# Kernel tuning notes

Hardware: AMD Instinct MI355X
Metric: run time of the kernel (lower is better)

The kernel has to match this reference:

```python
import jax, jax.numpy as jnp
import numpy as np


def _chamfer_sq(points, gts):
    # points: [B,N,3], gts: [B,M,3]
    pn = jnp.sum(points * points, axis=-1)              # [B,N]
    gn = jnp.sum(gts * gts, axis=-1)                    # [B,M]
    cross = jnp.einsum('bnd,bmd->bnm', points, gts)     # [B,N,M]
    d = pn[:, :, None] + gn[:, None, :] - 2.0 * cross   # [B,N,M]
    d = jnp.maximum(d, 0.0)
    p2g = jnp.min(d, axis=2)                            # [B,N] squared NN dist
    g2p = jnp.min(d, axis=1)                            # [B,M]
    return p2g, g2p


def setup_inputs() -> dict:
    key = jax.random.key(0)
    k1, k2 = jax.random.split(key)
    B, N, M = 8, 4096, 4096
    points = jax.random.normal(k1, (B, N, 3), dtype=jnp.float32)
    gts = jax.random.normal(k2, (B, M, 3), dtype=jnp.float32)
    return {"points": points, "gts": gts}


def reference(points, gts):
    p2g_sq, g2p_sq = _chamfer_sq(points, gts)
    p2g = jnp.sqrt(jnp.mean(p2g_sq, axis=1))   # [B]
    g2p = jnp.sqrt(jnp.mean(g2p_sq, axis=1))   # [B]
    loss = (p2g + g2p) / 2.0
    return (jnp.mean(loss), jnp.mean(p2g), jnp.mean(g2p))
```

## Files before the change

kernel.cpp:

```cpp
#include <hip/hip_runtime.h>
#include <math.h>

#define NPTS 4096
#define NB   8
#define QCB  512
#define RCB  1024
#define NQC  (NPTS / QCB)
#define NRC  (NPTS / RCB)

typedef _Float16 h8     __attribute__((ext_vector_type(8)));
typedef float    f32x16 __attribute__((ext_vector_type(16)));

#define FOREACH_T(OP) OP(0) OP(1) OP(2) OP(3)

__device__ __forceinline__ void split2(float v, _Float16& h, _Float16& l) {
    h = (_Float16)v;
    l = (_Float16)(v - (float)h);
}

__global__ __launch_bounds__(256, 2) void chamfer_mfma32(
    const float* __restrict__ P, const float* __restrict__ G,
    float* __restrict__ qpart,
    float* __restrict__ rpart,
    int* __restrict__ counter)
{
    __shared__ __align__(16) unsigned char smem[32768];
    h8*    Bfr = (h8*)smem;
    float* qtr = (float*)smem;

    const int dir = blockIdx.z;
    const int b   = blockIdx.y;
    const int qc  = blockIdx.x >> 2;
    const int rc  = blockIdx.x & 3;
    const int tid = threadIdx.x;
    const int w    = tid >> 6;
    const int lane = tid & 63;
    const int col  = lane & 31;
    const int kg   = lane >> 5;

    if (blockIdx.x == 0 && b == 0 && dir == 0 && tid == 0) *counter = 0;

    const float* __restrict__ Qb = (dir ? G : P) + (size_t)b * NPTS * 3;
    const float* __restrict__ Rb = (dir ? P : G) + (size_t)b * NPTS * 3;

    const _Float16 one = (_Float16)1.f, zr = (_Float16)0.f;

#pragma unroll
    for (int i = 0; i < 8; ++i) {
        const int e    = tid + i * 256;
        const int el   = e & 63;
        const int ecol = el & 31, ekg = el >> 5;
        const int ref  = rc * RCB + (e >> 6) * 32 + ecol;
        const float gx = Rb[3 * ref], gy = Rb[3 * ref + 1], gz = Rb[3 * ref + 2];
        const float gn = fmaf(gx, gx, fmaf(gy, gy, gz * gz));
        _Float16 xh, xl, yh, yl, zh, zl, nh, nl;
        split2(gx, xh, xl); split2(gy, yh, yl); split2(gz, zh, zl); split2(gn, nh, nl);
        Bfr[e] = ekg ? (h8){one, nh, xl, yl, zl, zr, nl, zr}
                     : (h8){xh, yh, zh, one, nh, xh, yh, zh};
    }

#define DECLT(t) h8 afr##t; f32x16 qa##t;
    FOREACH_T(DECLT)
#undef DECLT
#define MKA(t) { \
        const int q0 = qc * QCB + w * 128 + (t) * 32 + col;                   \
        const float px = Qb[3 * q0], py = Qb[3 * q0 + 1], pz = Qb[3 * q0 + 2];\
        const float m2x = -2.f * px, m2y = -2.f * py, m2z = -2.f * pz;        \
        const float pn = fmaf(px, px, fmaf(py, py, pz * pz));                 \
        _Float16 xh, xl, yh, yl, zh, zl, ph, pl;                              \
        split2(m2x, xh, xl); split2(m2y, yh, yl); split2(m2z, zh, zl);        \
        split2(pn, ph, pl);                                                   \
        afr##t = kg ? (h8){pl, zr, xh, yh, zh, ph, one, zr}                   \
                    : (h8){xh, yh, zh, ph, one, xl, yl, zl};                  \
        _Pragma("unroll")                                                     \
        for (int j = 0; j < 16; ++j) qa##t[j] = 3.4e38f; }
    FOREACH_T(MKA)
#undef MKA

    __syncthreads();

    const f32x16 cz = (f32x16){0.f,0.f,0.f,0.f,0.f,0.f,0.f,0.f,
                               0.f,0.f,0.f,0.f,0.f,0.f,0.f,0.f};
#pragma unroll 2
    for (int rt = 0; rt < 32; ++rt) {
        const h8 bfr = Bfr[rt * 64 + lane];
#define DOT(t) { \
        f32x16 d = __builtin_amdgcn_mfma_f32_32x32x16_f16(afr##t, bfr, cz, 0, 0, 0); \
        _Pragma("unroll")                                                     \
        for (int j = 0; j < 16; ++j) qa##t[j] = fminf(qa##t[j], d[j]); }
        FOREACH_T(DOT)
#undef DOT
    }

    __syncthreads();

    float* qw = qtr + w * 1088;
    float* outb = (dir ? rpart : qpart)
                + ((size_t)b * NRC + rc) * NPTS + qc * QCB + w * 128;
#define EPI(t) { \
        _Pragma("unroll")                                                     \
        for (int j = 0; j < 16; ++j) {                                        \
            const int row = (j & 3) + 8 * (j >> 2) + 4 * kg;                  \
            qw[row * 34 + col] = qa##t[j];                                    \
        }                                                                     \
        if (lane < 32) {                                                      \
            const float2* qr = (const float2*)(qw + lane * 34);               \
            float m = 3.4e38f;                                                \
            _Pragma("unroll")                                                 \
            for (int k = 0; k < 16; ++k) {                                    \
                float2 u = qr[k];                                             \
                m = fminf(m, fminf(u.x, u.y));                                \
            }                                                                 \
            outb[(t) * 32 + lane] = fmaxf(m, 0.f);                            \
        } }
    FOREACH_T(EPI)
#undef EPI
}

__global__ __launch_bounds__(256) void chamfer_reduce2(
    const float* __restrict__ qpart, const float* __restrict__ rpart,
    float* __restrict__ sums, int* __restrict__ counter, float* __restrict__ out)
{
    const int t  = blockIdx.x >> 2;
    const int sp = blockIdx.x & 3;
    const float* __restrict__ base =
        (t >= 8 ? rpart + (size_t)(t - 8) * NRC * NPTS
                : qpart + (size_t)t * NRC * NPTS);

    float sum = 0.f;
#pragma unroll
    for (int i = 0; i < 4; ++i) {
        const int q = sp * 1024 + i * 256 + threadIdx.x;
        float mn = base[q];
#pragma unroll
        for (int c = 1; c < NRC; ++c) mn = fminf(mn, base[(size_t)c * NPTS + q]);
        sum += mn;
    }

    __shared__ float red[256];
    __shared__ int amLast;
    red[threadIdx.x] = sum;
    __syncthreads();
    if (threadIdx.x < 128) red[threadIdx.x] += red[threadIdx.x + 128];
    __syncthreads();
    if (threadIdx.x < 64) {
        float v = red[threadIdx.x] + red[threadIdx.x + 64];
#pragma unroll
        for (int off = 32; off > 0; off >>= 1) v += __shfl_down(v, off, 64);
        if (threadIdx.x == 0) {
            sums[blockIdx.x] = v;
            __threadfence();
            amLast = (atomicAdd(counter, 1) == 63);
        }
    }
    __syncthreads();

    if (amLast) {
        __shared__ float r16[16];
        if (threadIdx.x < 16) {
            float acc = 0.f;
#pragma unroll
            for (int k = 0; k < 4; ++k)
                acc += *(volatile const float*)&sums[threadIdx.x * 4 + k];
            r16[threadIdx.x] = sqrtf(acc / (float)NPTS);
        }
        __syncthreads();
        if (threadIdx.x == 0) {
            float p2g = 0.f, g2p = 0.f;
#pragma unroll
            for (int bb = 0; bb < NB; ++bb) { p2g += r16[bb]; g2p += r16[NB + bb]; }
            p2g *= (1.0f / NB);
            g2p *= (1.0f / NB);
            out[0] = 0.5f * (p2g + g2p);
            out[1] = p2g;
            out[2] = g2p;
            *counter = 0;
        }
    }
}

extern "C" void kernel_launch(void* const* d_in, const int* in_sizes, int n_in,
                              void* d_out, int out_size, void* d_ws, size_t ws_size,
                              hipStream_t stream) {
    const float* points = (const float*)d_in[0];
    const float* gts    = (const float*)d_in[1];
    float* out = (float*)d_out;

    float* qpart = (float*)d_ws;
    float* rpart = qpart + (size_t)NB * NRC * NPTS;
    float* sums  = rpart + (size_t)NB * NRC * NPTS;
    int*   counter = (int*)(sums + 64);

    dim3 grid1(NQC * NRC, NB, 2);
    chamfer_mfma32<<<grid1, 256, 0, stream>>>(points, gts, qpart, rpart, counter);

    chamfer_reduce2<<<dim3(64), 256, 0, stream>>>(qpart, rpart, sums, counter, out);
}
```

Baseline: 22.43 us.

## Fuse partial-min reduction into main kernel via last-block-per-group atomic counters

Removes the separate reduction kernel launch. Each block atomically increments a counter for its (direction, batch) group. The last-arriving block combines that group's partial minima and sums them, and a second counter picks the final block to write the scalar outputs. In exchange, a hipMemsetAsync on the counters is added before launch, and each group's reduction now runs serially in a single block instead of being spread over 4 blocks.

```diff
diff --git a/kernel.cpp b/kernel.cpp
--- a/kernel.cpp
+++ b/kernel.cpp
@@ -7,6 +7,7 @@
 #define RCB  1024
 #define NQC  (NPTS / QCB)
 #define NRC  (NPTS / RCB)
+#define GRP  (NQC * NRC)
 
 typedef _Float16 h8     __attribute__((ext_vector_type(8)));
 typedef float    f32x16 __attribute__((ext_vector_type(16)));
@@ -18,11 +19,14 @@
     l = (_Float16)(v - (float)h);
 }
 
-__global__ __launch_bounds__(256, 2) void chamfer_mfma32(
+__global__ __launch_bounds__(256, 2) void chamfer_fused(
     const float* __restrict__ P, const float* __restrict__ G,
     float* __restrict__ qpart,
     float* __restrict__ rpart,
-    int* __restrict__ counter)
+    int* __restrict__ gctr,
+    int* __restrict__ fctr,
+    float* __restrict__ gsum,
+    float* __restrict__ out)
 {
     __shared__ __align__(16) unsigned char smem[32768];
     h8*    Bfr = (h8*)smem;
@@ -37,8 +41,6 @@
     const int lane = tid & 63;
     const int col  = lane & 31;
     const int kg   = lane >> 5;
-
-    if (blockIdx.x == 0 && b == 0 && dir == 0 && tid == 0) *counter = 0;
 
     const float* __restrict__ Qb = (dir ? G : P) + (size_t)b * NPTS * 3;
     const float* __restrict__ Rb = (dir ? P : G) + (size_t)b * NPTS * 3;
@@ -115,57 +117,50 @@
         } }
     FOREACH_T(EPI)
 #undef EPI
-}
 
-__global__ __launch_bounds__(256) void chamfer_reduce2(
-    const float* __restrict__ qpart, const float* __restrict__ rpart,
-    float* __restrict__ sums, int* __restrict__ counter, float* __restrict__ out)
-{
-    const int t  = blockIdx.x >> 2;
-    const int sp = blockIdx.x & 3;
-    const float* __restrict__ base =
-        (t >= 8 ? rpart + (size_t)(t - 8) * NRC * NPTS
-                : qpart + (size_t)t * NRC * NPTS);
+    __threadfence();
+    __shared__ int amLastS;
+    const int g = dir * NB + b;
+    if (tid == 0) amLastS = (atomicAdd(&gctr[g], 1) == GRP - 1);
+    __syncthreads();
+    if (!amLastS) return;
 
-    float sum = 0.f;
+    {
+        const float* __restrict__ base =
+            (dir ? rpart : qpart) + (size_t)b * NRC * NPTS;
+        float sum = 0.f;
+#pragma unroll 4
+        for (int i = 0; i < NPTS / 256; ++i) {
+            const int q = i * 256 + tid;
+            float mn = base[q];
 #pragma unroll
-    for (int i = 0; i < 4; ++i) {
-        const int q = sp * 1024 + i * 256 + threadIdx.x;
-        float mn = base[q];
+            for (int c = 1; c < NRC; ++c) mn = fminf(mn, base[(size_t)c * NPTS + q]);
+            sum += mn;
+        }
+        float* red = (float*)smem;
+        red[tid] = sum;
+        __syncthreads();
+        if (tid < 128) red[tid] += red[tid + 128];
+        __syncthreads();
+        __shared__ int amFinalS;
+        if (tid < 64) {
+            float v = red[tid] + red[tid + 64];
 #pragma unroll
-        for (int c = 1; c < NRC; ++c) mn = fminf(mn, base[(size_t)c * NPTS + q]);
-        sum += mn;
-    }
-
-    __shared__ float red[256];
-    __shared__ int amLast;
-    red[threadIdx.x] = sum;
-    __syncthreads();
-    if (threadIdx.x < 128) red[threadIdx.x] += red[threadIdx.x + 128];
-    __syncthreads();
-    if (threadIdx.x < 64) {
-        float v = red[threadIdx.x] + red[threadIdx.x + 64];
-#pragma unroll
-        for (int off = 32; off > 0; off >>= 1) v += __shfl_down(v, off, 64);
-        if (threadIdx.x == 0) {
-            sums[blockIdx.x] = v;
-            __threadfence();
-            amLast = (atomicAdd(counter, 1) == 63);
-        }
-    }
-    __syncthreads();
-
-    if (amLast) {
-        __shared__ float r16[16];
-        if (threadIdx.x < 16) {
-            float acc = 0.f;
-#pragma unroll
-            for (int k = 0; k < 4; ++k)
-                acc += *(volatile const float*)&sums[threadIdx.x * 4 + k];
-            r16[threadIdx.x] = sqrtf(acc / (float)NPTS);
+            for (int off = 32; off > 0; off >>= 1) v += __shfl_down(v, off, 64);
+            if (tid == 0) {
+                gsum[g] = v;
+                __threadfence();
+                amFinalS = (atomicAdd(fctr, 1) == 2 * NB - 1);
+            }
         }
         __syncthreads();
-        if (threadIdx.x == 0) {
+        if (!amFinalS) return;
+
+        __shared__ float r16[16];
+        if (tid < 16)
+            r16[tid] = sqrtf(*(volatile const float*)&gsum[tid] / (float)NPTS);
+        __syncthreads();
+        if (tid == 0) {
             float p2g = 0.f, g2p = 0.f;
 #pragma unroll
             for (int bb = 0; bb < NB; ++bb) { p2g += r16[bb]; g2p += r16[NB + bb]; }
@@ -174,7 +169,6 @@
             out[0] = 0.5f * (p2g + g2p);
             out[1] = p2g;
             out[2] = g2p;
-            *counter = 0;
         }
     }
 }
@@ -188,11 +182,13 @@
 
     float* qpart = (float*)d_ws;
     float* rpart = qpart + (size_t)NB * NRC * NPTS;
-    float* sums  = rpart + (size_t)NB * NRC * NPTS;
-    int*   counter = (int*)(sums + 64);
+    float* gsum  = rpart + (size_t)NB * NRC * NPTS;
+    int*   gctr  = (int*)(gsum + 16);
+    int*   fctr  = gctr + 16;
+
+    hipMemsetAsync(gctr, 0, 17 * sizeof(int), stream);
 
     dim3 grid1(NQC * NRC, NB, 2);
-    chamfer_mfma32<<<grid1, 256, 0, stream>>>(points, gts, qpart, rpart, counter);
-
-    chamfer_reduce2<<<dim3(64), 256, 0, stream>>>(qpart, rpart, sums, counter, out);
+    chamfer_fused<<<grid1, 256, 0, stream>>>(points, gts, qpart, rpart,
+                                             gctr, fctr, gsum, out);
 }
```

Measured after the change: 61.40 us. 174% more time.

## Compute both chamfer directions from one distance pass using LDS atomicMin column reductions

Applied to the files above, without the earlier changes.

The kernel used to launch a second grid dimension that recomputed the full distance matrix with points and ground truth swapped. It now computes each tile once and takes both the row minima (points to gts) and the column minima (gts to points). Column minima are combined across lanes and waves through integer atomicMin on a shared buffer. That is valid because the values are clamped non-negative, so their float bit patterns order the same as integers. The block grows to 512 threads over a 512x512 tile, and the reduction kernel now merges 8 partial slices in each direction. This halves the MFMA work in exchange for extra in-loop min trees and LDS atomics, which could contend.

```diff
diff --git a/kernel.cpp b/kernel.cpp
--- a/kernel.cpp
+++ b/kernel.cpp
@@ -3,55 +3,56 @@
 
 #define NPTS 4096
 #define NB   8
+#define BLK  512
 #define QCB  512
-#define RCB  1024
+#define RCB  512
 #define NQC  (NPTS / QCB)
 #define NRC  (NPTS / RCB)
+#define NRT  (RCB / 32)
 
 typedef _Float16 h8     __attribute__((ext_vector_type(8)));
 typedef float    f32x16 __attribute__((ext_vector_type(16)));
-
-#define FOREACH_T(OP) OP(0) OP(1) OP(2) OP(3)
 
 __device__ __forceinline__ void split2(float v, _Float16& h, _Float16& l) {
     h = (_Float16)v;
     l = (_Float16)(v - (float)h);
 }
 
-__global__ __launch_bounds__(256, 2) void chamfer_mfma32(
+__global__ __launch_bounds__(BLK, 2) void chamfer_mfma32(
     const float* __restrict__ P, const float* __restrict__ G,
     float* __restrict__ qpart,
     float* __restrict__ rpart,
     int* __restrict__ counter)
 {
-    __shared__ __align__(16) unsigned char smem[32768];
-    h8*    Bfr = (h8*)smem;
-    float* qtr = (float*)smem;
-
-    const int dir = blockIdx.z;
+    __shared__ __align__(16) unsigned char smem[34816];
+    h8*    Bfr  = (h8*)smem;
+    int*   rbuf = (int*)(smem + 16384);
+    float* qtr  = (float*)smem;
+
     const int b   = blockIdx.y;
-    const int qc  = blockIdx.x >> 2;
-    const int rc  = blockIdx.x & 3;
+    const int qc  = blockIdx.x >> 3;
+    const int rc  = blockIdx.x & 7;
     const int tid = threadIdx.x;
     const int w    = tid >> 6;
     const int lane = tid & 63;
     const int col  = lane & 31;
     const int kg   = lane >> 5;
 
-    if (blockIdx.x == 0 && b == 0 && dir == 0 && tid == 0) *counter = 0;
-
-    const float* __restrict__ Qb = (dir ? G : P) + (size_t)b * NPTS * 3;
-    const float* __restrict__ Rb = (dir ? P : G) + (size_t)b * NPTS * 3;
+    if (blockIdx.x == 0 && b == 0 && tid == 0) *counter = 0;
+
+    const float* __restrict__ Pb = P + (size_t)b * NPTS * 3;
+    const float* __restrict__ Gb = G + (size_t)b * NPTS * 3;
 
     const _Float16 one = (_Float16)1.f, zr = (_Float16)0.f;
 
-#pragma unroll
-    for (int i = 0; i < 8; ++i) {
-        const int e    = tid + i * 256;
+    if (tid < RCB) rbuf[tid] = 0x7f7fffff;
+#pragma unroll
+    for (int i = 0; i < 2; ++i) {
+        const int e    = tid + i * BLK;
         const int el   = e & 63;
         const int ecol = el & 31, ekg = el >> 5;
         const int ref  = rc * RCB + (e >> 6) * 32 + ecol;
-        const float gx = Rb[3 * ref], gy = Rb[3 * ref + 1], gz = Rb[3 * ref + 2];
+        const float gx = Gb[3 * ref], gy = Gb[3 * ref + 1], gz = Gb[3 * ref + 2];
         const float gn = fmaf(gx, gx, fmaf(gy, gy, gz * gz));
         _Float16 xh, xl, yh, yl, zh, zl, nh, nl;
         split2(gx, xh, xl); split2(gy, yh, yl); split2(gz, zh, zl); split2(gn, nh, nl);
@@ -59,12 +60,13 @@
                      : (h8){xh, yh, zh, one, nh, xh, yh, zh};
     }
 
+#define FOREACH_T(OP) OP(0) OP(1)
 #define DECLT(t) h8 afr##t; f32x16 qa##t;
     FOREACH_T(DECLT)
 #undef DECLT
 #define MKA(t) { \
-        const int q0 = qc * QCB + w * 128 + (t) * 32 + col;                   \
-        const float px = Qb[3 * q0], py = Qb[3 * q0 + 1], pz = Qb[3 * q0 + 2];\
+        const int q0 = qc * QCB + w * 64 + (t) * 32 + col;                    \
+        const float px = Pb[3 * q0], py = Pb[3 * q0 + 1], pz = Pb[3 * q0 + 2];\
         const float m2x = -2.f * px, m2y = -2.f * py, m2z = -2.f * pz;        \
         const float pn = fmaf(px, px, fmaf(py, py, pz * pz));                 \
         _Float16 xh, xl, yh, yl, zh, zl, ph, pl;                              \
@@ -82,26 +84,41 @@
     const f32x16 cz = (f32x16){0.f,0.f,0.f,0.f,0.f,0.f,0.f,0.f,
                                0.f,0.f,0.f,0.f,0.f,0.f,0.f,0.f};
 #pragma unroll 2
-    for (int rt = 0; rt < 32; ++rt) {
+    for (int rt = 0; rt < NRT; ++rt) {
         const h8 bfr = Bfr[rt * 64 + lane];
-#define DOT(t) { \
-        f32x16 d = __builtin_amdgcn_mfma_f32_32x32x16_f16(afr##t, bfr, cz, 0, 0, 0); \
-        _Pragma("unroll")                                                     \
-        for (int j = 0; j < 16; ++j) qa##t[j] = fminf(qa##t[j], d[j]); }
-        FOREACH_T(DOT)
-#undef DOT
-    }
-
+        f32x16 d0 = __builtin_amdgcn_mfma_f32_32x32x16_f16(afr0, bfr, cz, 0, 0, 0);
+        f32x16 d1 = __builtin_amdgcn_mfma_f32_32x32x16_f16(afr1, bfr, cz, 0, 0, 0);
+#pragma unroll
+        for (int j = 0; j < 16; ++j) qa0[j] = fminf(qa0[j], d0[j]);
+#pragma unroll
+        for (int j = 0; j < 16; ++j) qa1[j] = fminf(qa1[j], d1[j]);
+        float c0 = fminf(fminf(fminf(d0[0], d0[1]),  d0[2]),
+                         fminf(fminf(d0[3], d0[4]),  d0[5]));
+        float c1 = fminf(fminf(fminf(d0[6], d0[7]),  d0[8]),
+                         fminf(fminf(d0[9], d0[10]), d0[11]));
+        float c2 = fminf(fminf(fminf(d0[12], d0[13]), d0[14]), d0[15]);
+        float c3 = fminf(fminf(fminf(d1[0], d1[1]),  d1[2]),
+                         fminf(fminf(d1[3], d1[4]),  d1[5]));
+        float c4 = fminf(fminf(fminf(d1[6], d1[7]),  d1[8]),
+                         fminf(fminf(d1[9], d1[10]), d1[11]));
+        float c5 = fminf(fminf(fminf(d1[12], d1[13]), d1[14]), d1[15]);
+        float v  = fminf(fminf(fminf(c0, c1), c2), fminf(fminf(c3, c4), c5));
+        v = fmaxf(v, 0.f);
+        atomicMin(&rbuf[rt * 32 + col], __float_as_int(v));
+    }
+
+    __syncthreads();
+    if (tid < RCB)
+        rpart[((size_t)b * NQC + qc) * NPTS + rc * RCB + tid] = __int_as_float(rbuf[tid]);
     __syncthreads();
 
     float* qw = qtr + w * 1088;
-    float* outb = (dir ? rpart : qpart)
-                + ((size_t)b * NRC + rc) * NPTS + qc * QCB + w * 128;
-#define EPI(t) { \
+    float* outb = qpart + ((size_t)b * NRC + rc) * NPTS + qc * QCB + w * 64;
+#define EPI(t, QA) { \
         _Pragma("unroll")                                                     \
         for (int j = 0; j < 16; ++j) {                                        \
             const int row = (j & 3) + 8 * (j >> 2) + 4 * kg;                  \
-            qw[row * 34 + col] = qa##t[j];                                    \
+            qw[row * 34 + col] = QA[j];                                       \
         }                                                                     \
         if (lane < 32) {                                                      \
             const float2* qr = (const float2*)(qw + lane * 34);               \
@@ -113,7 +130,8 @@
             }                                                                 \
             outb[(t) * 32 + lane] = fmaxf(m, 0.f);                            \
         } }
-    FOREACH_T(EPI)
+    EPI(0, qa0)
+    EPI(1, qa1)
 #undef EPI
 }
 
@@ -124,8 +142,8 @@
     const int t  = blockIdx.x >> 2;
     const int sp = blockIdx.x & 3;
     const float* __restrict__ base =
-        (t >= 8 ? rpart + (size_t)(t - 8) * NRC * NPTS
-                : qpart + (size_t)t * NRC * NPTS);
+        (t >= 8 ? rpart + (size_t)(t - 8) * 8 * NPTS
+                : qpart + (size_t)t * 8 * NPTS);
 
     float sum = 0.f;
 #pragma unroll
@@ -133,7 +151,7 @@
         const int q = sp * 1024 + i * 256 + threadIdx.x;
         float mn = base[q];
 #pragma unroll
-        for (int c = 1; c < NRC; ++c) mn = fminf(mn, base[(size_t)c * NPTS + q]);
+        for (int c = 1; c < 8; ++c) mn = fminf(mn, base[(size_t)c * NPTS + q]);
         sum += mn;
     }
 
@@ -187,12 +205,12 @@
     float* out = (float*)d_out;
 
     float* qpart = (float*)d_ws;
-    float* rpart = qpart + (size_t)NB * NRC * NPTS;
-    float* sums  = rpart + (size_t)NB * NRC * NPTS;
+    float* rpart = qpart + (size_t)NB * 8 * NPTS;
+    float* sums  = rpart + (size_t)NB * 8 * NPTS;
     int*   counter = (int*)(sums + 64);
 
-    dim3 grid1(NQC * NRC, NB, 2);
-    chamfer_mfma32<<<grid1, 256, 0, stream>>>(points, gts, qpart, rpart, counter);
+    dim3 grid1(NQC * NRC, NB);
+    chamfer_mfma32<<<grid1, BLK, 0, stream>>>(points, gts, qpart, rpart, counter);
 
     chamfer_reduce2<<<dim3(64), 256, 0, stream>>>(qpart, rpart, sums, counter, out);
 }
```

Measured after the change: 21.15 us. 1.06x faster.

## Precompute fp16 split fragments in a prepass and swap MFMA operand roles

Applied to the files above, without the earlier changes.

A new prepass kernel converts both point sets once into hi/lo fp16 MFMA fragments in global memory, so the main kernel no longer repeats the per-block split and norm work. The main kernel swaps the operand roles so the queries sit along the accumulator's row dimension. Each lane then reduces its 16 outputs in registers and writes a per-half partial, which drops the shared-memory transpose epilogue. The reference chunk is smaller and the grid larger, and occupancy is raised. This costs an extra kernel launch and a larger partial buffer (16 slices per query) for the reduce kernel to read.

```diff
diff --git a/kernel.cpp b/kernel.cpp
--- a/kernel.cpp
+++ b/kernel.cpp
@@ -3,10 +3,11 @@
 
 #define NPTS 4096
 #define NB   8
-#define QCB  512
-#define RCB  1024
-#define NQC  (NPTS / QCB)
-#define NRC  (NPTS / RCB)
+#define QG   512
+#define RCC  512
+#define NQG  (NPTS / QG)
+#define NRC  (NPTS / RCC)
+#define T    4
 
 typedef _Float16 h8     __attribute__((ext_vector_type(8)));
 typedef float    f32x16 __attribute__((ext_vector_type(16)));
@@ -18,114 +19,104 @@
     l = (_Float16)(v - (float)h);
 }
 
-__global__ __launch_bounds__(256, 2) void chamfer_mfma32(
+__global__ __launch_bounds__(1024) void chamfer_frags(
     const float* __restrict__ P, const float* __restrict__ G,
-    float* __restrict__ qpart,
-    float* __restrict__ rpart,
-    int* __restrict__ counter)
+    h8* __restrict__ FA_P, h8* __restrict__ FB_P,
+    h8* __restrict__ FA_G, h8* __restrict__ FB_G, int* __restrict__ counter)
 {
-    __shared__ __align__(16) unsigned char smem[32768];
-    h8*    Bfr = (h8*)smem;
-    float* qtr = (float*)smem;
+    const int g = blockIdx.x * 1024 + threadIdx.x;
+    if (g == 0) *counter = 0;
+    const int set = g >> 15;
+    const int b   = (g >> 12) & 7;
+    const int i   = g & 4095;
+    const float* src = (set ? G : P) + ((size_t)b * NPTS + i) * 3;
+    const float x = src[0], y = src[1], z = src[2];
+    const float n = fmaf(x, x, fmaf(y, y, z * z));
+    const float m2x = -2.f * x, m2y = -2.f * y, m2z = -2.f * z;
+    const _Float16 one = (_Float16)1.f, zr = (_Float16)0.f;
+    _Float16 axh, axl, ayh, ayl, azh, azl, anh, anl;
+    split2(m2x, axh, axl); split2(m2y, ayh, ayl); split2(m2z, azh, azl);
+    split2(n, anh, anl);
+    _Float16 bxh, bxl, byh, byl, bzh, bzl;
+    split2(x, bxh, bxl); split2(y, byh, byl); split2(z, bzh, bzl);
 
-    const int dir = blockIdx.z;
-    const int b   = blockIdx.y;
-    const int qc  = blockIdx.x >> 2;
-    const int rc  = blockIdx.x & 3;
-    const int tid = threadIdx.x;
+    h8* FA = (set ? FA_G : FA_P) + (size_t)b * 2 * NPTS;
+    h8* FB = (set ? FB_G : FB_P) + (size_t)b * 2 * NPTS;
+    FA[i]        = (h8){axh, ayh, azh, anh, one, axl, ayl, azl};
+    FA[NPTS + i] = (h8){anl, zr, axh, ayh, azh, anh, one, zr};
+    FB[i]        = (h8){bxh, byh, bzh, one, anh, bxh, byh, bzh};
+    FB[NPTS + i] = (h8){one, anh, bxl, byl, bzl, zr, anl, zr};
+}
+
+__global__ __launch_bounds__(256, 4) void chamfer_mfma32(
+    const h8* __restrict__ FA_P, const h8* __restrict__ FB_P,
+    const h8* __restrict__ FA_G, const h8* __restrict__ FB_G,
+    float* __restrict__ part)
+{
+    __shared__ h8 Alds[2][RCC];
+
+    const int pass = blockIdx.z;
+    const int b    = blockIdx.y;
+    const int qg   = blockIdx.x >> 3;
+    const int rc   = blockIdx.x & 7;
+    const int tid  = threadIdx.x;
     const int w    = tid >> 6;
     const int lane = tid & 63;
     const int col  = lane & 31;
     const int kg   = lane >> 5;
 
-    if (blockIdx.x == 0 && b == 0 && dir == 0 && tid == 0) *counter = 0;
-
-    const float* __restrict__ Qb = (dir ? G : P) + (size_t)b * NPTS * 3;
-    const float* __restrict__ Rb = (dir ? P : G) + (size_t)b * NPTS * 3;
-
-    const _Float16 one = (_Float16)1.f, zr = (_Float16)0.f;
+    const h8* __restrict__ FA = (pass ? FA_P : FA_G) + (size_t)b * 2 * NPTS;
+    const h8* __restrict__ FB = (pass ? FB_G : FB_P) + (size_t)b * 2 * NPTS;
 
 #pragma unroll
-    for (int i = 0; i < 8; ++i) {
-        const int e    = tid + i * 256;
-        const int el   = e & 63;
-        const int ecol = el & 31, ekg = el >> 5;
-        const int ref  = rc * RCB + (e >> 6) * 32 + ecol;
-        const float gx = Rb[3 * ref], gy = Rb[3 * ref + 1], gz = Rb[3 * ref + 2];
-        const float gn = fmaf(gx, gx, fmaf(gy, gy, gz * gz));
-        _Float16 xh, xl, yh, yl, zh, zl, nh, nl;
-        split2(gx, xh, xl); split2(gy, yh, yl); split2(gz, zh, zl); split2(gn, nh, nl);
-        Bfr[e] = ekg ? (h8){one, nh, xl, yl, zl, zr, nl, zr}
-                     : (h8){xh, yh, zh, one, nh, xh, yh, zh};
+    for (int i = 0; i < 4; ++i) {
+        const int e   = tid + i * 256;
+        const int ekg = e >> 9, le = e & 511;
+        Alds[ekg][le] = FA[(size_t)ekg * NPTS + rc * RCC + le];
     }
 
-#define DECLT(t) h8 afr##t; f32x16 qa##t;
+    const int qb = qg * QG + w * (T * 32);
+#define DECLT(t) h8 bf##t; float acc##t;
     FOREACH_T(DECLT)
 #undef DECLT
-#define MKA(t) { \
-        const int q0 = qc * QCB + w * 128 + (t) * 32 + col;                   \
-        const float px = Qb[3 * q0], py = Qb[3 * q0 + 1], pz = Qb[3 * q0 + 2];\
-        const float m2x = -2.f * px, m2y = -2.f * py, m2z = -2.f * pz;        \
-        const float pn = fmaf(px, px, fmaf(py, py, pz * pz));                 \
-        _Float16 xh, xl, yh, yl, zh, zl, ph, pl;                              \
-        split2(m2x, xh, xl); split2(m2y, yh, yl); split2(m2z, zh, zl);        \
-        split2(pn, ph, pl);                                                   \
-        afr##t = kg ? (h8){pl, zr, xh, yh, zh, ph, one, zr}                   \
-                    : (h8){xh, yh, zh, ph, one, xl, yl, zl};                  \
-        _Pragma("unroll")                                                     \
-        for (int j = 0; j < 16; ++j) qa##t[j] = 3.4e38f; }
-    FOREACH_T(MKA)
-#undef MKA
+#define LOADB(t) bf##t = FB[(size_t)kg * NPTS + qb + (t) * 32 + col]; acc##t = 3.4e38f;
+    FOREACH_T(LOADB)
+#undef LOADB
 
     __syncthreads();
 
     const f32x16 cz = (f32x16){0.f,0.f,0.f,0.f,0.f,0.f,0.f,0.f,
                                0.f,0.f,0.f,0.f,0.f,0.f,0.f,0.f};
-#pragma unroll 2
-    for (int rt = 0; rt < 32; ++rt) {
-        const h8 bfr = Bfr[rt * 64 + lane];
+#pragma unroll 4
+    for (int rt = 0; rt < RCC / 32; ++rt) {
+        const h8 a = Alds[kg][rt * 32 + col];
 #define DOT(t) { \
-        f32x16 d = __builtin_amdgcn_mfma_f32_32x32x16_f16(afr##t, bfr, cz, 0, 0, 0); \
-        _Pragma("unroll")                                                     \
-        for (int j = 0; j < 16; ++j) qa##t[j] = fminf(qa##t[j], d[j]); }
+        f32x16 d = __builtin_amdgcn_mfma_f32_32x32x16_f16(a, bf##t, cz, 0, 0, 0); \
+        float t0 = fminf(fminf(d[0],  d[1]),  d[2]);                          \
+        float t1 = fminf(fminf(d[3],  d[4]),  d[5]);                          \
+        float t2 = fminf(fminf(d[6],  d[7]),  d[8]);                          \
+        float t3 = fminf(fminf(d[9],  d[10]), d[11]);                         \
+        float t4 = fminf(fminf(d[12], d[13]), d[14]);                         \
+        float u0 = fminf(fminf(t0, t1), t2);                                  \
+        float u1 = fminf(fminf(t3, t4), d[15]);                               \
+        acc##t = fminf(fminf(u0, u1), acc##t); }
         FOREACH_T(DOT)
 #undef DOT
     }
 
-    __syncthreads();
-
-    float* qw = qtr + w * 1088;
-    float* outb = (dir ? rpart : qpart)
-                + ((size_t)b * NRC + rc) * NPTS + qc * QCB + w * 128;
-#define EPI(t) { \
-        _Pragma("unroll")                                                     \
-        for (int j = 0; j < 16; ++j) {                                        \
-            const int row = (j & 3) + 8 * (j >> 2) + 4 * kg;                  \
-            qw[row * 34 + col] = qa##t[j];                                    \
-        }                                                                     \
-        if (lane < 32) {                                                      \
-            const float2* qr = (const float2*)(qw + lane * 34);               \
-            float m = 3.4e38f;                                                \
-            _Pragma("unroll")                                                 \
-            for (int k = 0; k < 16; ++k) {                                    \
-                float2 u = qr[k];                                             \
-                m = fminf(m, fminf(u.x, u.y));                                \
-            }                                                                 \
-            outb[(t) * 32 + lane] = fmaxf(m, 0.f);                            \
-        } }
-    FOREACH_T(EPI)
-#undef EPI
+    float* outb = part + (((size_t)(pass * NB + b)) * 16 + rc * 2 + kg) * NPTS + qb;
+#define STORET(t) outb[(t) * 32 + col] = fmaxf(acc##t, 0.f);
+    FOREACH_T(STORET)
+#undef STORET
 }
 
 __global__ __launch_bounds__(256) void chamfer_reduce2(
-    const float* __restrict__ qpart, const float* __restrict__ rpart,
+    const float* __restrict__ part,
     float* __restrict__ sums, int* __restrict__ counter, float* __restrict__ out)
 {
     const int t  = blockIdx.x >> 2;
     const int sp = blockIdx.x & 3;
-    const float* __restrict__ base =
-        (t >= 8 ? rpart + (size_t)(t - 8) * NRC * NPTS
-                : qpart + (size_t)t * NRC * NPTS);
+    const float* __restrict__ base = part + (size_t)t * 16 * NPTS;
 
     float sum = 0.f;
 #pragma unroll
@@ -133,8 +124,8 @@
         const int q = sp * 1024 + i * 256 + threadIdx.x;
         float mn = base[q];
 #pragma unroll
-        for (int c = 1; c < NRC; ++c) mn = fminf(mn, base[(size_t)c * NPTS + q]);
-        sum += mn;
+        for (int c = 1; c < 16; ++c) mn = fminf(mn, base[(size_t)c * NPTS + q]);
+        sum += fmaxf(mn, 0.f);
     }
 
     __shared__ float red[256];
@@ -186,13 +177,20 @@
     const float* gts    = (const float*)d_in[1];
     float* out = (float*)d_out;
 
-    float* qpart = (float*)d_ws;
-    float* rpart = qpart + (size_t)NB * NRC * NPTS;
-    float* sums  = rpart + (size_t)NB * NRC * NPTS;
+    const size_t FRAG = (size_t)NB * 2 * NPTS;
+    h8* FA_P = (h8*)d_ws;
+    h8* FB_P = FA_P + FRAG;
+    h8* FA_G = FB_P + FRAG;
+    h8* FB_G = FA_G + FRAG;
+    float* part = (float*)(FB_G + FRAG);
+    float* sums = part + (size_t)2 * NB * 16 * NPTS;
     int*   counter = (int*)(sums + 64);
 
-    dim3 grid1(NQC * NRC, NB, 2);
-    chamfer_mfma32<<<grid1, 256, 0, stream>>>(points, gts, qpart, rpart, counter);
+    chamfer_frags<<<dim3(64), 1024, 0, stream>>>(points, gts,
+                                                 FA_P, FB_P, FA_G, FB_G, counter);
 
-    chamfer_reduce2<<<dim3(64), 256, 0, stream>>>(qpart, rpart, sums, counter, out);
+    dim3 grid1(NQG * NRC, NB, 2);
+    chamfer_mfma32<<<grid1, 256, 0, stream>>>(FA_P, FB_P, FA_G, FB_G, part);
+
+    chamfer_reduce2<<<dim3(64), 256, 0, stream>>>(part, sums, counter, out);
 }
```

After: 26.81 us. 1.2x slower.
